# Kernel optimization log

Hardware: AMD Instinct MI355X
Metric: run time of the kernel (lower is better)

The kernel has to match this reference:

```python
import jax, jax.numpy as jnp
import numpy as np

T, B, IN, H, OUT = 512, 256, 64, 1024, 1


def setup_inputs() -> dict:
    key = jax.random.key(0)
    ks = jax.random.split(key, 12)
    s = 1.0 / np.sqrt(H)
    u = lambda k, shape: jax.random.uniform(k, shape, jnp.float32, -s, s)
    return {
        "x": jax.random.normal(ks[0], (T, B, IN), jnp.float32),
        # LSTMCell 1 (input -> hidden); gate order i, f, g, o (PyTorch)
        "W_ih1": u(ks[1], (4 * H, IN)),
        "W_hh1": u(ks[2], (4 * H, H)),
        "b_ih1": u(ks[3], (4 * H,)),
        "b_hh1": u(ks[4], (4 * H,)),
        # LSTMCell 2 (hidden -> hidden)
        "W_ih2": u(ks[5], (4 * H, H)),
        "W_hh2": u(ks[6], (4 * H, H)),
        "b_ih2": u(ks[7], (4 * H,)),
        "b_hh2": u(ks[8], (4 * H,)),
        # l2: Linear(hidden -> output). NOTE: l1 exists in the module but is
        # never used in forward, so it is omitted here.
        "W2": u(ks[9], (OUT, H)),
        "b2": u(ks[10], (OUT,)),
    }


def _lstm_cell(x_t, h, c, W_ih, W_hh, b_ih, b_hh):
    # gates: [B, 4H], PyTorch gate order (i, f, g, o)
    g = x_t @ W_ih.T + h @ W_hh.T + (b_ih + b_hh)
    i, f, gg, o = jnp.split(g, 4, axis=-1)
    c_new = jax.nn.sigmoid(f) * c + jax.nn.sigmoid(i) * jnp.tanh(gg)
    h_new = jax.nn.sigmoid(o) * jnp.tanh(c_new)
    return h_new, c_new


def reference(x, W_ih1, W_hh1, b_ih1, b_hh1, W_ih2, W_hh2, b_ih2, b_hh2, W2, b2):
    Tn, Bn = x.shape[0], x.shape[1]
    Hn = W_hh1.shape[1]
    z = jnp.zeros((Bn, Hn), x.dtype)

    def step(carry, x_t):
        h1, c1, h2, c2 = carry
        h1, c1 = _lstm_cell(x_t, h1, c1, W_ih1, W_hh1, b_ih1, b_hh1)
        h2, c2 = _lstm_cell(h1, h2, c2, W_ih2, W_hh2, b_ih2, b_hh2)
        y = jax.nn.sigmoid(h2 @ W2.T + b2)  # [B, OUT]
        return (h1, c1, h2, c2), y

    _, ys = jax.lax.scan(step, (z, z, z, z), x)
    return ys  # [T, B, OUT] == torch.stack(res)
```

## Files before the change

### kernel.cpp

```cpp
#include <hip/hip_runtime.h>
#include <stdint.h>


#define TT   512
#define BAT  256
#define INP  64
#define HID  1024
#define KA   1088
#define KB   2048
#define SZH  (BAT*HID)
#define NBLK 256
#define NTHR 256

typedef __attribute__((ext_vector_type(8))) short bf16x8;
typedef __attribute__((ext_vector_type(4))) float f32x4;

#define OFF_BA   0ull
#define OFF_BB   8912896ull
#define OFF_XB   25690112ull
#define OFF_H1   42467328ull
#define OFF_H2   43515904ull
#define OFF_Y    44564480ull
#define OFF_B1P  48758784ull
#define OFF_B2P  48775168ull
#define OFF_BAR  48791552ull
#define WS_END   48799744ull

__device__ __forceinline__ unsigned short f2bf(float f) {
  unsigned u = __float_as_uint(f);
  u += 0x7FFFu + ((u >> 16) & 1u);
  return (unsigned short)(u >> 16);
}
__device__ __forceinline__ float sigm_(float x) { return 1.0f / (1.0f + __expf(-x)); }
__device__ __forceinline__ float tanh_(float x) {
  float t = __expf(-2.0f * fabsf(x));
  float r = (1.0f - t) / (1.0f + t);
  return x < 0.0f ? -r : r;
}
__device__ __forceinline__ f32x4 mfma16(bf16x8 a, bf16x8 b, f32x4 c) {
  return __builtin_amdgcn_mfma_f32_16x16x32_bf16(a, b, c, 0, 0, 0);
}

__device__ __forceinline__ void group_barrier(unsigned* bar, unsigned phase, int m, int leaf) {
  __syncthreads();
  if (threadIdx.x == 0) {
    __builtin_amdgcn_fence(__ATOMIC_RELEASE, "agent");
    unsigned* lp = bar + (m * 16 + leaf) * 32;
    unsigned* rp = bar + (m * 16 + 8) * 32;
    unsigned old = __hip_atomic_fetch_add(lp, 1u, __ATOMIC_RELAXED, __HIP_MEMORY_SCOPE_AGENT);
    if (old + 1u == phase * 8u)
      __hip_atomic_fetch_add(rp, 1u, __ATOMIC_RELAXED, __HIP_MEMORY_SCOPE_AGENT);
    unsigned tgt = phase * 8u;
    int spins = 0;
    while (__hip_atomic_load(rp, __ATOMIC_RELAXED, __HIP_MEMORY_SCOPE_AGENT) < tgt) {
      __builtin_amdgcn_s_sleep(2);
      if (++spins > (1 << 17)) break;
    }
    __builtin_amdgcn_fence(__ATOMIC_ACQUIRE, "agent");
  }
  __syncthreads();
}

__global__ void k_zero(unsigned* __restrict__ p, long n) {
  long i = (long)blockIdx.x * blockDim.x + threadIdx.x;
  long s = (long)gridDim.x * blockDim.x;
  for (; i < n; i += s) p[i] = 0u;
}

__global__ void k_packw(const float* __restrict__ Wih, const float* __restrict__ Whh,
                        unsigned short* __restrict__ out, int kih, int K) {
  int i = blockIdx.x * blockDim.x + threadIdx.x;
  int n = 4096 * K;
  int stride = gridDim.x * blockDim.x;
  for (; i < n; i += stride) {
    int p = i / K, k = i - p * K;
    int bh = p >> 6, g = (p >> 4) & 3, h = p & 15;
    int wrow = g * HID + bh * 16 + h;
    float v = (k < kih) ? Wih[(size_t)wrow * kih + k] : Whh[(size_t)wrow * HID + (k - kih)];
    out[i] = f2bf(v);
  }
}

__global__ void k_convx(const float* __restrict__ x, unsigned short* __restrict__ xb) {
  int i = blockIdx.x * blockDim.x + threadIdx.x;
  int stride = gridDim.x * blockDim.x;
  for (; i < TT * BAT * INP; i += stride) xb[i] = f2bf(x[i]);
}

__global__ void k_bias(const float* __restrict__ bih1, const float* __restrict__ bhh1,
                       const float* __restrict__ bih2, const float* __restrict__ bhh2,
                       float* __restrict__ b1p, float* __restrict__ b2p) {
  int p = blockIdx.x * blockDim.x + threadIdx.x;
  if (p < 4096) {
    int bh = p >> 6, g = (p >> 4) & 3, h = p & 15;
    int wrow = g * HID + bh * 16 + h;
    b1p[p] = bih1[wrow] + bhh1[wrow];
    b2p[p] = bih2[wrow] + bhh2[wrow];
  }
}

__global__ __launch_bounds__(NTHR, 1) void k_lstm(
    const unsigned short* __restrict__ BA, const unsigned short* __restrict__ BB,
    const unsigned short* __restrict__ XB,
    unsigned short* __restrict__ H1, unsigned short* __restrict__ H2,
    const float* __restrict__ B1P, const float* __restrict__ B2P,
    const float* __restrict__ W2, float* __restrict__ YACC,
    unsigned* __restrict__ BAR)
{
  __shared__ bf16x8 W1L[34 * 4 * 4 * 16];
  __shared__ f32x4  BUF[4 * 4 * 4 * 16];

  const int bid = blockIdx.x;
  const int s = bid & 1;
  const int m = (bid & 7) >> 1;
  const int bh = (bid >> 3) | (s << 5);
  const int leaf = s * 4 + ((bid >> 3) & 3);
  const int tid = threadIdx.x;
  const int lane = tid & 63, wave = tid >> 6;
  const int l15 = lane & 15, kq = lane >> 4;
  const int grow0 = m * 64 + wave * 16;
  const int arow = grow0 + l15;
  const int hcol = bh * 16 + l15;
  const int colb = bh * 64;

  {
    const int kq2 = tid >> 6, g2 = (tid >> 4) & 3, l2 = tid & 15;
    for (int c = 0; c < 34; ++c) {
      const bf16x8* src = (const bf16x8*)(BA + (size_t)(colb + g2 * 16 + l2) * KA);
      W1L[((c * 4 + kq2) * 4 + g2) * 16 + l2] = src[c * 4 + kq2];
    }
  }
  bf16x8 w2r[16][4];
#pragma unroll
  for (int g = 0; g < 4; ++g) {
    const bf16x8* src = (const bf16x8*)(BB + (size_t)(colb + g * 16 + l15) * KB);
#pragma unroll
    for (int cc = 0; cc < 16; ++cc) w2r[cc][g] = src[(wave * 16 + cc) * 4 + kq];
  }
  const float ba0 = B1P[colb + l15], ba1 = B1P[colb + 16 + l15],
              ba2 = B1P[colb + 32 + l15], ba3 = B1P[colb + 48 + l15];
  const float bb0 = B2P[colb + l15], bb1 = B2P[colb + 16 + l15],
              bb2 = B2P[colb + 32 + l15], bb3 = B2P[colb + 48 + l15];
  const float w2v = W2[hcol];
  float c1r[4] = {0.f, 0.f, 0.f, 0.f};
  float c2r[4] = {0.f, 0.f, 0.f, 0.f};
  __syncthreads();

  for (int p = 0; p <= TT; ++p) {
    const int cur = p & 1, prv = cur ^ 1;

    if (p < TT) {
      f32x4 acc1[4];
#pragma unroll
      for (int g = 0; g < 4; ++g) acc1[g] = (f32x4){0.f, 0.f, 0.f, 0.f};
      const bf16x8* xf  = (const bf16x8*)XB + ((size_t)p * BAT + arow) * 8;
      const bf16x8* h1f = (const bf16x8*)(H1 + (size_t)prv * SZH) + (size_t)arow * 128;
#pragma unroll
      for (int c = 0; c < 34; ++c) {
        bf16x8 a = (c < 2) ? xf[c * 4 + kq] : h1f[(c - 2) * 4 + kq];
#pragma unroll
        for (int g = 0; g < 4; ++g)
          acc1[g] = mfma16(a, W1L[((c * 4 + kq) * 4 + g) * 16 + l15], acc1[g]);
      }
      unsigned short* h1w = H1 + (size_t)cur * SZH;
#pragma unroll
      for (int j = 0; j < 4; ++j) {
        float gi = acc1[0][j] + ba0, gf = acc1[1][j] + ba1,
              gg = acc1[2][j] + ba2, go = acc1[3][j] + ba3;
        float cn = sigm_(gf) * c1r[j] + sigm_(gi) * tanh_(gg);
        float hn = sigm_(go) * tanh_(cn);
        c1r[j] = cn;
        h1w[(size_t)(grow0 + kq * 4 + j) * HID + hcol] = f2bf(hn);
      }
    }

    if (p >= 1) {
      f32x4 acc2[4][4];
#pragma unroll
      for (int i = 0; i < 4; ++i)
#pragma unroll
        for (int g = 0; g < 4; ++g) acc2[i][g] = (f32x4){0.f, 0.f, 0.f, 0.f};
      const bf16x8* af = (wave < 2) ? (const bf16x8*)(H1 + (size_t)prv * SZH)
                                    : (const bf16x8*)(H2 + (size_t)cur * SZH);
      const int fo = (wave < 2) ? wave * 64 : (wave - 2) * 64;
#pragma unroll
      for (int cc = 0; cc < 16; ++cc) {
        bf16x8 afr[4];
#pragma unroll
        for (int i = 0; i < 4; ++i)
          afr[i] = af[(size_t)(m * 64 + i * 16 + l15) * 128 + fo + cc * 4 + kq];
#pragma unroll
        for (int i = 0; i < 4; ++i)
#pragma unroll
          for (int g = 0; g < 4; ++g) acc2[i][g] = mfma16(afr[i], w2r[cc][g], acc2[i][g]);
      }

#pragma unroll
      for (int d = 1; d < 4; ++d) {
#pragma unroll
        for (int t = 0; t < 4; ++t) {
          if (((wave + d) & 3) == t) {
#pragma unroll
            for (int g = 0; g < 4; ++g)
              BUF[((wave * 4 + g) * 4 + kq) * 16 + l15] = acc2[t][g];
          }
        }
        __syncthreads();
#pragma unroll
        for (int t = 0; t < 4; ++t) {
          if (wave == t) {
            const int rs = (t - d) & 3;
#pragma unroll
            for (int g = 0; g < 4; ++g)
              acc2[t][g] += BUF[((rs * 4 + g) * 4 + kq) * 16 + l15];
          }
        }
        if (d < 3) __syncthreads();
      }

      unsigned short* h2w = H2 + (size_t)prv * SZH;
      f32x4 g0, g1, g2, g3;
#pragma unroll
      for (int t = 0; t < 4; ++t)
        if (wave == t) { g0 = acc2[t][0]; g1 = acc2[t][1]; g2 = acc2[t][2]; g3 = acc2[t][3]; }
#pragma unroll
      for (int j = 0; j < 4; ++j) {
        float gi = g0[j] + bb0, gf = g1[j] + bb1, gg = g2[j] + bb2, go = g3[j] + bb3;
        float cn = sigm_(gf) * c2r[j] + sigm_(gi) * tanh_(gg);
        float hn = sigm_(go) * tanh_(cn);
        c2r[j] = cn;
        int gr = grow0 + kq * 4 + j;
        h2w[(size_t)gr * HID + hcol] = f2bf(hn);
        float v = hn * w2v;
        v += __shfl_xor(v, 1);
        v += __shfl_xor(v, 2);
        v += __shfl_xor(v, 4);
        v += __shfl_xor(v, 8);
        if (l15 == 0) atomicAdd(YACC + ((size_t)(p - 1) * BAT + gr) * 8 + ((bid >> 3) & 7), v);
      }
    }

    if (p < TT) group_barrier(BAR, (unsigned)(p + 1), m, leaf);
  }
}

__global__ void k_fin(const float* __restrict__ yacc, const float* __restrict__ b2,
                      float* __restrict__ out) {
  int i = blockIdx.x * blockDim.x + threadIdx.x;
  if (i < TT * BAT) {
    const float* y = yacc + (size_t)i * 8;
    float a = (y[0] + y[1]) + (y[2] + y[3]) + ((y[4] + y[5]) + (y[6] + y[7]));
    out[i] = 1.0f / (1.0f + __expf(-(a + b2[0])));
  }
}

extern "C" void kernel_launch(void* const* d_in, const int* in_sizes, int n_in,
                              void* d_out, int out_size, void* d_ws, size_t ws_size,
                              hipStream_t stream) {
  const float* x    = (const float*)d_in[0];
  const float* Wih1 = (const float*)d_in[1];
  const float* Whh1 = (const float*)d_in[2];
  const float* bih1 = (const float*)d_in[3];
  const float* bhh1 = (const float*)d_in[4];
  const float* Wih2 = (const float*)d_in[5];
  const float* Whh2 = (const float*)d_in[6];
  const float* bih2 = (const float*)d_in[7];
  const float* bhh2 = (const float*)d_in[8];
  const float* W2   = (const float*)d_in[9];
  const float* b2   = (const float*)d_in[10];
  (void)in_sizes; (void)n_in; (void)out_size; (void)ws_size;

  char* ws = (char*)d_ws;
  unsigned short* BA  = (unsigned short*)(ws + OFF_BA);
  unsigned short* BBp = (unsigned short*)(ws + OFF_BB);
  unsigned short* XBp = (unsigned short*)(ws + OFF_XB);
  unsigned short* H1  = (unsigned short*)(ws + OFF_H1);
  unsigned short* H2  = (unsigned short*)(ws + OFF_H2);
  float* YACC = (float*)(ws + OFF_Y);
  float* B1P  = (float*)(ws + OFF_B1P);
  float* B2P  = (float*)(ws + OFF_B2P);
  unsigned* BAR = (unsigned*)(ws + OFF_BAR);

  k_zero<<<512, 256, 0, stream>>>((unsigned*)(ws + OFF_H1), (long)((WS_END - OFF_H1) / 4));
  k_packw<<<1024, 256, 0, stream>>>(Wih1, Whh1, BA, INP, KA);
  k_packw<<<2048, 256, 0, stream>>>(Wih2, Whh2, BBp, HID, KB);
  k_convx<<<1024, 256, 0, stream>>>(x, XBp);
  k_bias<<<16, 256, 0, stream>>>(bih1, bhh1, bih2, bhh2, B1P, B2P);
  k_lstm<<<NBLK, NTHR, 0, stream>>>(BA, BBp, XBp, H1, H2, B1P, B2P, W2, YACC, BAR);
  k_fin<<<512, 256, 0, stream>>>(YACC, b2, (float*)d_out);
}
```

Measured before the change: 15.23 ms.

## Double waves per block and split K across wave pairs in LSTM kernel

Raises the persistent LSTM kernel from 4 to 8 waves per block. Each pair of waves splits the K dimension of both the layer-1 and layer-2 GEMMs, and the partial sums are combined through shared memory before the gate nonlinearities. The aim is more latency hiding and fewer weight registers per wave (w2r is halved). The cost is extra __syncthreads and LDS reduction passes every timestep, and only half the waves run the elementwise epilogue.

```diff
diff --git a/kernel.cpp b/kernel.cpp
--- a/kernel.cpp
+++ b/kernel.cpp
@@ -10,7 +10,7 @@
 #define KB   2048
 #define SZH  (BAT*HID)
 #define NBLK 256
-#define NTHR 256
+#define NTHR 512
 
 typedef __attribute__((ext_vector_type(8))) short bf16x8;
 typedef __attribute__((ext_vector_type(4))) float f32x4;
@@ -99,7 +99,7 @@
   }
 }
 
-__global__ __launch_bounds__(NTHR, 1) void k_lstm(
+__global__ __launch_bounds__(NTHR, 2) void k_lstm(
     const unsigned short* __restrict__ BA, const unsigned short* __restrict__ BB,
     const unsigned short* __restrict__ XB,
     unsigned short* __restrict__ H1, unsigned short* __restrict__ H2,
@@ -118,24 +118,22 @@
   const int tid = threadIdx.x;
   const int lane = tid & 63, wave = tid >> 6;
   const int l15 = lane & 15, kq = lane >> 4;
-  const int grow0 = m * 64 + wave * 16;
+  const int r4 = wave & 3, k2 = wave >> 2;
+  const int grow0 = m * 64 + r4 * 16;
   const int arow = grow0 + l15;
   const int hcol = bh * 16 + l15;
   const int colb = bh * 64;
 
-  {
-    const int kq2 = tid >> 6, g2 = (tid >> 4) & 3, l2 = tid & 15;
-    for (int c = 0; c < 34; ++c) {
-      const bf16x8* src = (const bf16x8*)(BA + (size_t)(colb + g2 * 16 + l2) * KA);
-      W1L[((c * 4 + kq2) * 4 + g2) * 16 + l2] = src[c * 4 + kq2];
-    }
-  }
-  bf16x8 w2r[16][4];
+  for (int i = tid; i < 34 * 256; i += NTHR) {
+    const int c = i >> 8, kqq = (i >> 6) & 3, g = (i >> 4) & 3, l = i & 15;
+    W1L[i] = ((const bf16x8*)(BA + (size_t)(colb + g * 16 + l) * KA))[c * 4 + kqq];
+  }
+  bf16x8 w2r[8][4];
 #pragma unroll
   for (int g = 0; g < 4; ++g) {
     const bf16x8* src = (const bf16x8*)(BB + (size_t)(colb + g * 16 + l15) * KB);
 #pragma unroll
-    for (int cc = 0; cc < 16; ++cc) w2r[cc][g] = src[(wave * 16 + cc) * 4 + kq];
+    for (int cc = 0; cc < 8; ++cc) w2r[cc][g] = src[(wave * 8 + cc) * 4 + kq];
   }
   const float ba0 = B1P[colb + l15], ba1 = B1P[colb + 16 + l15],
               ba2 = B1P[colb + 32 + l15], ba3 = B1P[colb + 48 + l15];
@@ -155,23 +153,37 @@
       for (int g = 0; g < 4; ++g) acc1[g] = (f32x4){0.f, 0.f, 0.f, 0.f};
       const bf16x8* xf  = (const bf16x8*)XB + ((size_t)p * BAT + arow) * 8;
       const bf16x8* h1f = (const bf16x8*)(H1 + (size_t)prv * SZH) + (size_t)arow * 128;
-#pragma unroll
-      for (int c = 0; c < 34; ++c) {
+      const int cbeg = k2 * 17;
+#pragma unroll
+      for (int ci = 0; ci < 17; ++ci) {
+        const int c = cbeg + ci;
         bf16x8 a = (c < 2) ? xf[c * 4 + kq] : h1f[(c - 2) * 4 + kq];
 #pragma unroll
         for (int g = 0; g < 4; ++g)
           acc1[g] = mfma16(a, W1L[((c * 4 + kq) * 4 + g) * 16 + l15], acc1[g]);
       }
-      unsigned short* h1w = H1 + (size_t)cur * SZH;
-#pragma unroll
-      for (int j = 0; j < 4; ++j) {
-        float gi = acc1[0][j] + ba0, gf = acc1[1][j] + ba1,
-              gg = acc1[2][j] + ba2, go = acc1[3][j] + ba3;
-        float cn = sigm_(gf) * c1r[j] + sigm_(gi) * tanh_(gg);
-        float hn = sigm_(go) * tanh_(cn);
-        c1r[j] = cn;
-        h1w[(size_t)(grow0 + kq * 4 + j) * HID + hcol] = f2bf(hn);
-      }
+      if (k2 == 1) {
+#pragma unroll
+        for (int g = 0; g < 4; ++g)
+          BUF[((r4 * 4 + g) * 4 + kq) * 16 + l15] = acc1[g];
+      }
+      __syncthreads();
+      if (k2 == 0) {
+#pragma unroll
+        for (int g = 0; g < 4; ++g)
+          acc1[g] += BUF[((r4 * 4 + g) * 4 + kq) * 16 + l15];
+        unsigned short* h1w = H1 + (size_t)cur * SZH;
+#pragma unroll
+        for (int j = 0; j < 4; ++j) {
+          float gi = acc1[0][j] + ba0, gf = acc1[1][j] + ba1,
+                gg = acc1[2][j] + ba2, go = acc1[3][j] + ba3;
+          float cn = sigm_(gf) * c1r[j] + sigm_(gi) * tanh_(gg);
+          float hn = sigm_(go) * tanh_(cn);
+          c1r[j] = cn;
+          h1w[(size_t)(grow0 + kq * 4 + j) * HID + hcol] = f2bf(hn);
+        }
+      }
+      __syncthreads();
     }
 
     if (p >= 1) {
@@ -180,11 +192,11 @@
       for (int i = 0; i < 4; ++i)
 #pragma unroll
         for (int g = 0; g < 4; ++g) acc2[i][g] = (f32x4){0.f, 0.f, 0.f, 0.f};
-      const bf16x8* af = (wave < 2) ? (const bf16x8*)(H1 + (size_t)prv * SZH)
+      const bf16x8* af = (wave < 4) ? (const bf16x8*)(H1 + (size_t)prv * SZH)
                                     : (const bf16x8*)(H2 + (size_t)cur * SZH);
-      const int fo = (wave < 2) ? wave * 64 : (wave - 2) * 64;
-#pragma unroll
-      for (int cc = 0; cc < 16; ++cc) {
+      const int fo = (wave < 4 ? wave : wave - 4) * 32;
+#pragma unroll
+      for (int cc = 0; cc < 8; ++cc) {
         bf16x8 afr[4];
 #pragma unroll
         for (int i = 0; i < 4; ++i)
@@ -196,10 +208,26 @@
       }
 
 #pragma unroll
+      for (int t = 0; t < 4; ++t) {
+        if (wave >= 4) {
+#pragma unroll
+          for (int g = 0; g < 4; ++g)
+            BUF[(((wave - 4) * 4 + g) * 4 + kq) * 16 + l15] = acc2[t][g];
+        }
+        __syncthreads();
+        if (wave < 4) {
+#pragma unroll
+          for (int g = 0; g < 4; ++g)
+            acc2[t][g] += BUF[((wave * 4 + g) * 4 + kq) * 16 + l15];
+        }
+        __syncthreads();
+      }
+
+#pragma unroll
       for (int d = 1; d < 4; ++d) {
 #pragma unroll
         for (int t = 0; t < 4; ++t) {
-          if (((wave + d) & 3) == t) {
+          if (wave < 4 && ((wave + d) & 3) == t) {
 #pragma unroll
             for (int g = 0; g < 4; ++g)
               BUF[((wave * 4 + g) * 4 + kq) * 16 + l15] = acc2[t][g];
@@ -218,25 +246,27 @@
         if (d < 3) __syncthreads();
       }
 
-      unsigned short* h2w = H2 + (size_t)prv * SZH;
-      f32x4 g0, g1, g2, g3;
-#pragma unroll
-      for (int t = 0; t < 4; ++t)
-        if (wave == t) { g0 = acc2[t][0]; g1 = acc2[t][1]; g2 = acc2[t][2]; g3 = acc2[t][3]; }
-#pragma unroll
-      for (int j = 0; j < 4; ++j) {
-        float gi = g0[j] + bb0, gf = g1[j] + bb1, gg = g2[j] + bb2, go = g3[j] + bb3;
-        float cn = sigm_(gf) * c2r[j] + sigm_(gi) * tanh_(gg);
-        float hn = sigm_(go) * tanh_(cn);
-        c2r[j] = cn;
-        int gr = grow0 + kq * 4 + j;
-        h2w[(size_t)gr * HID + hcol] = f2bf(hn);
-        float v = hn * w2v;
-        v += __shfl_xor(v, 1);
-        v += __shfl_xor(v, 2);
-        v += __shfl_xor(v, 4);
-        v += __shfl_xor(v, 8);
-        if (l15 == 0) atomicAdd(YACC + ((size_t)(p - 1) * BAT + gr) * 8 + ((bid >> 3) & 7), v);
+      if (wave < 4) {
+        unsigned short* h2w = H2 + (size_t)prv * SZH;
+        f32x4 g0, g1, g2, g3;
+#pragma unroll
+        for (int t = 0; t < 4; ++t)
+          if (wave == t) { g0 = acc2[t][0]; g1 = acc2[t][1]; g2 = acc2[t][2]; g3 = acc2[t][3]; }
+#pragma unroll
+        for (int j = 0; j < 4; ++j) {
+          float gi = g0[j] + bb0, gf = g1[j] + bb1, gg = g2[j] + bb2, go = g3[j] + bb3;
+          float cn = sigm_(gf) * c2r[j] + sigm_(gi) * tanh_(gg);
+          float hn = sigm_(go) * tanh_(cn);
+          c2r[j] = cn;
+          int gr = grow0 + kq * 4 + j;
+          h2w[(size_t)gr * HID + hcol] = f2bf(hn);
+          float v = hn * w2v;
+          v += __shfl_xor(v, 1);
+          v += __shfl_xor(v, 2);
+          v += __shfl_xor(v, 4);
+          v += __shfl_xor(v, 8);
+          if (l15 == 0) atomicAdd(YACC + ((size_t)(p - 1) * BAT + gr) * 8 + ((bid >> 3) & 7), v);
+        }
       }
     }
 
```

After: 18.18 ms. 19.4% more time.
